# Performance work log

Hardware: AMD Instinct MI355X
Metric: run time of the kernel (lower is better)

## Reference

```python
import jax, jax.numpy as jnp
import numpy as np

# dims
B_, DM, DI, DS, DTR, DT_, G_, E_, K_, DC = 512, 1024, 2048, 64, 64, 64, 8, 4, 2, 4
# B_ batch, DM d_model, DI d_inner (expand*d_model), DS d_state, DTR dt_rank,
# DT_ D_time, G_ KAN grid size, E_ num_experts, K_ top_k, DC d_conv


def setup_inputs() -> dict:
    key = jax.random.key(0)
    ks = jax.random.split(key, 16)
    def n(i, shape, s=0.02):
        return jax.random.normal(ks[i], shape, dtype=jnp.float32) * s
    return {
        "uk_current_input": jax.random.normal(ks[0], (B_, DM), dtype=jnp.float32),
        "tk_current": jax.random.uniform(ks[1], (B_, 1), dtype=jnp.float32),
        "tk_previous": jax.random.uniform(ks[2], (B_, 1), dtype=jnp.float32),
        # input_proj
        "W_in": n(3, (DM, DM)), "b_in": jnp.zeros((DM,), jnp.float32),
        # K_MOTE router + sinusoidal time experts
        "router_W": n(4, (E_, 1), 1.0), "router_b": jnp.zeros((E_,), jnp.float32),
        "freq": jax.random.uniform(ks[5], (E_, DT_), minval=0.1, maxval=10.0),
        "phase": n(6, (E_, DT_), 1.0),
        "kan_W": n(7, (DT_, DT_, G_), 0.1),
        # Mamba SSM params
        "W_inproj": n(8, (2 * DI, DM)),
        "conv_w": n(9, (DI, DC), 0.1), "conv_b": jnp.zeros((DI,), jnp.float32),
        "W_x": n(10, (DTR + 2 * DS, DI)),
        "W_dt": n(11, (DI, DTR)), "dt_bias": jnp.full((DI,), -4.0, jnp.float32),
        "W_delta": n(12, (DI, DT_)),
        "A_log": jnp.log(jnp.tile(jnp.arange(1, DS + 1, dtype=jnp.float32), (DI, 1))),
        "D_skip": jnp.ones((DI,), jnp.float32),
        "W_out": n(13, (DM, DI)),
    }


def _k_mote(t, router_W, router_b, freq, phase):
    # t: (B,1) -> embedding (B, D_time), weights (B,E), mask (B,E)
    logits = t @ router_W.T + router_b                      # (B,E)
    w = jax.nn.softmax(logits, axis=-1)
    _, top_idx = jax.lax.top_k(w, K_)
    mask = jax.nn.one_hot(top_idx, E_, dtype=w.dtype).sum(axis=1)  # (B,E) binary
    w_sel = w * mask
    w_norm = w_sel / (w_sel.sum(axis=-1, keepdims=True) + 1e-8)
    # expert sinusoidal embeddings: (B,E,D_time)
    emb = jnp.sin(t[:, :, None] * freq[None] + phase[None])
    out = jnp.einsum('be,bed->bd', w_norm, emb)
    return out, w, mask


def _kan(x, kan_W):
    # rkhs_gaussian basis on fixed grid in [-1,1]
    grid = jnp.linspace(-1.0, 1.0, G_, dtype=x.dtype)
    h = 2.0 / (G_ - 1)
    phi = jnp.exp(-jnp.square((x[..., None] - grid) / h))   # (B, D_time, G)
    return jnp.einsum('big,oig->bo', phi, kan_W)


def _mamba_step(u, dt_emb, W_inproj, conv_w, conv_b, W_x, W_dt, dt_bias,
                W_delta, A_log, D_skip, W_out):
    # single-timestep selective scan (seq_len=1, zero initial state)
    xz = u @ W_inproj.T                                     # (B, 2*DI)
    x, z = jnp.split(xz, 2, axis=-1)
    # causal depthwise conv over a length-1 sequence with zero left-pad:
    # only the last kernel tap contributes
    x = x * conv_w[:, -1] + conv_b
    x = jax.nn.silu(x)
    x_dbl = x @ W_x.T                                       # (B, DTR+2*DS)
    dt_r = x_dbl[:, :DTR]
    Bmat = x_dbl[:, DTR:DTR + DS]                           # (B, DS)
    Cmat = x_dbl[:, DTR + DS:]                              # (B, DS)
    # dt modulated by the K-MOTE/KAN delta-time embedding
    dt = jax.nn.softplus(dt_r @ W_dt.T + dt_emb @ W_delta.T + dt_bias)  # (B, DI)
    # h_prev = 0 so exp(dt*A)*h_prev vanishes; h = (dt*B) * x
    h = (dt * x)[:, :, None] * Bmat[:, None, :]             # (B, DI, DS)
    y = jnp.einsum('bds,bs->bd', h, Cmat) + D_skip * x
    y = y * jax.nn.silu(z)
    return y @ W_out.T                                      # (B, DM)


def reference(uk_current_input, tk_current, tk_previous, W_in, b_in,
              router_W, router_b, freq, phase, kan_W, W_inproj, conv_w, conv_b,
              W_x, W_dt, dt_bias, W_delta, A_log, D_skip, W_out):
    processed_uk = uk_current_input @ W_in.T + b_in
    emb_tk, expert_weights, expert_mask = _k_mote(tk_current, router_W, router_b, freq, phase)
    emb_tk_prev, _, _ = _k_mote(tk_previous, router_W, router_b, freq, phase)
    delta_t_emb = _kan(emb_tk, kan_W) - _kan(emb_tk_prev, kan_W)
    hk = _mamba_step(processed_uk, delta_t_emb, W_inproj, conv_w, conv_b,
                     W_x, W_dt, dt_bias, W_delta, A_log, D_skip, W_out)
    return hk, expert_weights, expert_mask
```

## Files before the change

kernel.cpp:

```cpp
#include <hip/hip_runtime.h>
#include <hip/hip_bf16.h>
#include <math.h>

#define B_  512
#define DM  1024
#define DI  2048
#define DS  64
#define DTR 64
#define DT  64
#define G_  8
#define E_  4
#define DC  4

typedef __bf16 bf16x8 __attribute__((ext_vector_type(8)));
typedef float  f32x4  __attribute__((ext_vector_type(4)));
typedef unsigned short ushort_t;

__device__ __forceinline__ float bf2f(__hip_bfloat16 h) { return __bfloat162float(h); }
__device__ __forceinline__ __hip_bfloat16 f2bf(float f) { return __float2bfloat16(f); }
__device__ __forceinline__ float sigmoidf_(float x){ return 1.f/(1.f+expf(-x)); }
__device__ __forceinline__ float siluf_(float x){ return x*sigmoidf_(x); }
__device__ __forceinline__ float softplusf_(float x){ return (x>20.f)? x : log1pf(expf(x)); }

__device__ __forceinline__ unsigned int pack2(float a, float b) {
  unsigned short ua = __builtin_bit_cast(unsigned short, (__bf16)a);
  unsigned short ub = __builtin_bit_cast(unsigned short, (__bf16)b);
  return (unsigned int)ua | ((unsigned int)ub << 16);
}
__device__ __forceinline__ uint4 cvt8(float4 v0, float4 v1) {
  uint4 r;
  r.x = pack2(v0.x, v0.y); r.y = pack2(v0.z, v0.w);
  r.z = pack2(v1.x, v1.y); r.w = pack2(v1.z, v1.w);
  return r;
}

enum EpiKind { EPI_PART=0, EPI_G2=1, EPI_G4=2 };

struct KParams {
  const float *uk, *tk_c, *tk_p, *W_in, *b_in, *rW, *rb, *freq, *phase, *kanW;
  const float *W_inproj, *conv_w, *conv_b, *W_x, *W_dt, *dt_bias, *W_delta, *D_skip, *W_out;
  __hip_bfloat16 *Pu, *Xs, *Sz, *Yb, *Acat;
  __hip_bfloat16 *Wip_bf, *Wx_bf, *Wdt128, *Wout_bf;
  float *bc, *Part, *out_hk, *out_w, *out_mask;
};

__device__ __forceinline__ void cvt_chunk(const float* __restrict__ s,
                                          __hip_bfloat16* __restrict__ d)
{
  float4 v0 = *reinterpret_cast<const float4*>(s);
  float4 v1 = *reinterpret_cast<const float4*>(s + 4);
  *reinterpret_cast<uint4*>(d) = cvt8(v0, v1);
}

template<int BM, int BN, int WMT, int WNT, int EK, bool CVTA, bool CVTB>
__device__ __forceinline__ void gemm_tile(char* smemc, int bxi, int byi, int bzi,
    const void* __restrict__ Ap, const void* __restrict__ Bp,
    float* __restrict__ Coutp, int Ka, int Kb, int kLen, int N, const KParams& p)
{
  static_assert(BM == 32*WMT && BN == 32*WNT, "2x2 wave layout");
  constexpr int BK = 128, SA = 136;
  constexpr int NA = (BM*BK)/(256*8);
  constexpr int NB = (BN*BK)/(256*8);
  ushort_t* sA = (ushort_t*)smemc;
  ushort_t* sB = (ushort_t*)(smemc + (size_t)2*BM*SA*sizeof(ushort_t));
  const int tid  = threadIdx.x;
  const int wave = tid >> 6, lane = tid & 63;
  const int wm = wave >> 1, wn = wave & 1;
  const int r = lane & 15, q = lane >> 4;
  const int bm = byi * BM, bn = bxi * BN;
  const int kBase = bzi * kLen;
  const int T = kLen / BK;

  uint4 ua[NA], ub[NB];
  float4 fa[NA][2], fb[NB][2];

  auto loadTiles = [&](int k0) {
    #pragma unroll
    for (int c=0;c<NA;++c) {
      int idx = tid*8 + c*2048; int row = idx>>7, kk = idx&127;
      if constexpr (CVTA) {
        const float* s = (const float*)Ap + (size_t)(bm+row)*Ka + k0 + kk;
        fa[c][0] = *reinterpret_cast<const float4*>(s);
        fa[c][1] = *reinterpret_cast<const float4*>(s+4);
      } else {
        ua[c] = *reinterpret_cast<const uint4*>((const __hip_bfloat16*)Ap + (size_t)(bm+row)*Ka + k0 + kk);
      }
    }
    #pragma unroll
    for (int c=0;c<NB;++c) {
      int idx = tid*8 + c*2048; int row = idx>>7, kk = idx&127;
      if constexpr (CVTB) {
        const float* s = (const float*)Bp + (size_t)(bn+row)*Kb + k0 + kk;
        fb[c][0] = *reinterpret_cast<const float4*>(s);
        fb[c][1] = *reinterpret_cast<const float4*>(s+4);
      } else {
        ub[c] = *reinterpret_cast<const uint4*>((const __hip_bfloat16*)Bp + (size_t)(bn+row)*Kb + k0 + kk);
      }
    }
  };
  auto writeTiles = [&](int buf) {
    #pragma unroll
    for (int c=0;c<NA;++c) {
      int idx = tid*8 + c*2048; int row = idx>>7, kk = idx&127;
      uint4 v; if constexpr (CVTA) v = cvt8(fa[c][0], fa[c][1]); else v = ua[c];
      *reinterpret_cast<uint4*>(&sA[buf*(BM*SA) + row*SA + kk]) = v;
    }
    #pragma unroll
    for (int c=0;c<NB;++c) {
      int idx = tid*8 + c*2048; int row = idx>>7, kk = idx&127;
      uint4 v; if constexpr (CVTB) v = cvt8(fb[c][0], fb[c][1]); else v = ub[c];
      *reinterpret_cast<uint4*>(&sB[buf*(BN*SA) + row*SA + kk]) = v;
    }
  };

  f32x4 acc[WMT][WNT];
  #pragma unroll
  for (int i=0;i<WMT;++i)
    #pragma unroll
    for (int j=0;j<WNT;++j) acc[i][j] = (f32x4){0.f,0.f,0.f,0.f};

  loadTiles(kBase);
  writeTiles(0);
  for (int t=0; t<T; ++t) {
    __syncthreads();
    const int cur = t & 1;
    if (t+1 < T) loadTiles(kBase + (t+1)*BK);
    #pragma unroll
    for (int ks=0; ks<4; ++ks) {
      bf16x8 af[WMT], bfr[WNT];
      #pragma unroll
      for (int mt=0; mt<WMT; ++mt)
        af[mt] = *reinterpret_cast<const bf16x8*>(&sA[cur*(BM*SA) + (wm*(WMT*16)+mt*16+r)*SA + ks*32 + q*8]);
      #pragma unroll
      for (int nt=0; nt<WNT; ++nt)
        bfr[nt] = *reinterpret_cast<const bf16x8*>(&sB[cur*(BN*SA) + (wn*(WNT*16)+nt*16+r)*SA + ks*32 + q*8]);
      #pragma unroll
      for (int mt=0; mt<WMT; ++mt)
        #pragma unroll
        for (int nt=0; nt<WNT; ++nt)
          acc[mt][nt] = __builtin_amdgcn_mfma_f32_16x16x32_bf16(af[mt], bfr[nt], acc[mt][nt], 0,0,0);
    }
    if (t+1 < T) writeTiles(cur ^ 1);
  }

  #pragma unroll
  for (int mt=0; mt<WMT; ++mt) {
    #pragma unroll
    for (int nt=0; nt<WNT; ++nt) {
      #pragma unroll
      for (int i=0;i<4;++i) {
        int grow = bm + wm*(WMT*16) + mt*16 + q*4 + i;
        int gcol = bn + wn*(WNT*16) + nt*16 + r;
        float v = acc[mt][nt][i];
        if constexpr (EK == EPI_PART) {
          float* P = Coutp + (size_t)bzi * ((size_t)B_*N);
          P[(size_t)grow*N + gcol] = v;
        } else if constexpr (EK == EPI_G2) {
          if (gcol < DI) {
            float xc = v * p.conv_w[gcol*DC + (DC-1)] + p.conv_b[gcol];
            p.Xs[(size_t)grow*DI + gcol] = f2bf(siluf_(xc));
          } else {
            p.Sz[(size_t)grow*DI + (gcol - DI)] = f2bf(siluf_(v));
          }
        } else {
          float dt  = softplusf_(v + p.dt_bias[gcol]);
          float xsv = bf2f(p.Xs[(size_t)grow*DI + gcol]);
          float szv = bf2f(p.Sz[(size_t)grow*DI + gcol]);
          float y = (dt * xsv * p.bc[grow] + p.D_skip[gcol] * xsv) * szv;
          p.Yb[(size_t)grow*DI + gcol] = f2bf(y);
        }
      }
    }
  }
}


__device__ __forceinline__ void route(float t, const float* rW, const float* rb,
                                      float* w, float* mask, float* wn)
{
  float l[E_];
  float m = -1e30f;
  for (int e=0;e<E_;++e){ l[e] = t*rW[e] + rb[e]; m = fmaxf(m, l[e]); }
  float s = 0.f;
  for (int e=0;e<E_;++e){ w[e] = expf(l[e]-m); s += w[e]; }
  for (int e=0;e<E_;++e) w[e] /= s;
  int i1 = 0;
  for (int e=1;e<E_;++e) if (w[e] > w[i1]) i1 = e;
  int i2 = -1;
  for (int e=0;e<E_;++e) if (e != i1 && (i2 < 0 || w[e] > w[i2])) i2 = e;
  float ssel = w[i1] + w[i2] + 1e-8f;
  for (int e=0;e<E_;++e){
    float mk = (e==i1 || e==i2) ? 1.f : 0.f;
    mask[e] = mk;
    wn[e] = mk * w[e] / ssel;
  }
}

__device__ __forceinline__ void kan_job(char* smemc, int job, const KParams& p)
{
  float* dphi   = (float*)smemc;
  float* kchunk = dphi + 4*512;
  const int tid = threadIdx.x;
  const int wv = tid >> 6, lane = tid & 63;
  const int b = job*4 + wv;
  {
    float t  = p.tk_c[b];
    float tp = p.tk_p[b];
    float w_c[E_], mk_c[E_], wn_c[E_];
    float w_p[E_], mk_p[E_], wn_p[E_];
    route(t,  p.rW, p.rb, w_c, mk_c, wn_c);
    route(tp, p.rW, p.rb, w_p, mk_p, wn_p);
    if (lane < E_) {
      p.out_w[b*E_ + lane]    = w_c[lane];
      p.out_mask[b*E_ + lane] = mk_c[lane];
    }
    float ec = 0.f, epv = 0.f;
    #pragma unroll
    for (int e=0;e<E_;++e) {
      float f  = p.freq[e*DT + lane];
      float ph = p.phase[e*DT + lane];
      ec  += wn_c[e] * sinf(t*f + ph);
      epv += wn_p[e] * sinf(tp*f + ph);
    }
    const float h = 2.f/(G_-1);
    #pragma unroll
    for (int g=0; g<G_; ++g) {
      float gr = -1.f + g*h;
      float a  = (ec - gr)/h;
      float bb = (epv - gr)/h;
      dphi[wv*512 + lane*G_ + g] = expf(-a*a) - expf(-bb*bb);
    }
  }

  float accv = 0.f;
  #pragma unroll
  for (int c=0;c<4;++c) {
    __syncthreads();
    {
      const int rr = tid >> 2, seg = tid & 3;
      const float* src = p.kanW + (size_t)rr*512 + c*128 + seg*32;
      float* dst = kchunk + rr*132 + seg*32;
      #pragma unroll
      for (int i=0;i<8;++i)
        *reinterpret_cast<float4*>(dst + i*4) = *reinterpret_cast<const float4*>(src + i*4);
    }
    __syncthreads();
    const float* kr = kchunk + lane*132;
    const float* dd = dphi + wv*512 + c*128;
    #pragma unroll
    for (int j=0;j<128;j+=4) {
      float4 kv = *reinterpret_cast<const float4*>(kr + j);
      float4 dv = *reinterpret_cast<const float4*>(dd + j);
      accv += kv.x*dv.x + kv.y*dv.y + kv.z*dv.z + kv.w*dv.w;
    }
  }
  p.Acat[b*128 + 64 + lane] = f2bf(accv);
}


#define GEMM_SMEM(BM,BN) ((2*(BM)*136 + 2*(BN)*136)*2)

__global__ __launch_bounds__(256)
void g1kan_conv_kernel(KParams p)
{
  __shared__ __align__(16) char smem[GEMM_SMEM(32,64)];
  const int id = blockIdx.x, t = threadIdx.x;
  if (id < 128) {
    kan_job(smem, id, p);
  } else if (id < 1152) {
    const int id2 = id - 128;
    const int bxi = id2 & 15, byi = (id2 >> 4) & 15, bzi = id2 >> 8;
    gemm_tile<32,64,1,2,EPI_PART,true,true>(smem, bxi, byi, bzi,
        p.uk, p.W_in, p.Part, DM, DM, 256, DM, p);
  } else if (id < 3200) { size_t c = (size_t)(id-1152)*256 + t; cvt_chunk(p.W_inproj + c*8, p.Wip_bf  + c*8); }
  else if (id < 3392)   { size_t c = (size_t)(id-3200)*256 + t; cvt_chunk(p.W_x      + c*8, p.Wx_bf   + c*8); }
  else if (id < 4416)   { size_t c = (size_t)(id-3392)*256 + t; cvt_chunk(p.W_out    + c*8, p.Wout_bf + c*8); }
  else {                  size_t c = (size_t)(id-4416)*256 + t;
    int row = (int)(c >> 4), col0 = ((int)c & 15)*8;
    const float* s = (col0 < 64) ? (p.W_dt    + (size_t)row*64 + col0)
                                 : (p.W_delta + (size_t)row*64 + (col0-64));
    cvt_chunk(s, p.Wdt128 + (size_t)row*128 + col0);
  }
}

__global__ __launch_bounds__(256)
void g2_kernel(KParams p)
{
  __shared__ __align__(16) char smem[GEMM_SMEM(32,64)];
  const int bxi = blockIdx.x & 63, byi = blockIdx.x >> 6;
  gemm_tile<32,64,1,2,EPI_G2,false,false>(smem, bxi, byi, 0, p.Pu, p.Wip_bf, nullptr, DM, DM, DM, 2*DI, p);
}

__global__ __launch_bounds__(256)
void g3_kernel(KParams p)
{
  __shared__ __align__(16) char smem[GEMM_SMEM(32,64)];
  const int bxi = blockIdx.x % 3, rem = blockIdx.x / 3;
  const int byi = rem & 15, bzi = rem >> 4;
  gemm_tile<32,64,1,2,EPI_PART,false,false>(smem, bxi, byi, bzi, p.Xs, p.Wx_bf, p.Part, DI, DI, 256, 192, p);
}

__global__ __launch_bounds__(256)
void g4_kernel(KParams p)
{
  __shared__ __align__(16) char smem[GEMM_SMEM(32,64)];
  const int bxi = blockIdx.x & 31, byi = blockIdx.x >> 5;
  gemm_tile<32,64,1,2,EPI_G4,false,false>(smem, bxi, byi, 0, p.Acat, p.Wdt128, nullptr, 128, 128, 128, DI, p);
}

__global__ __launch_bounds__(256)
void g5_kernel(KParams p)
{
  __shared__ __align__(16) char smem[GEMM_SMEM(32,64)];
  const int bxi = blockIdx.x & 15, rem = blockIdx.x >> 4;
  const int byi = rem & 15, bzi = rem >> 4;
  gemm_tile<32,64,1,2,EPI_PART,false,false>(smem, bxi, byi, bzi, p.Yb, p.Wout_bf, p.Part, DI, DI, 512, DM, p);
}

__global__ __launch_bounds__(256)
void reduce_bias_kernel(KParams p)
{
  const int i = blockIdx.x*256 + threadIdx.x;
  const int total = B_*DM/4;
  const float4* pp = (const float4*)p.Part;
  float4 s = pp[i];
  #pragma unroll
  for (int k=1;k<4;++k){ float4 t = pp[i + k*total]; s.x+=t.x; s.y+=t.y; s.z+=t.z; s.w+=t.w; }
  float4 bv = ((const float4*)p.b_in)[i & (DM/4 - 1)];
  uint2 o; o.x = pack2(s.x+bv.x, s.y+bv.y); o.y = pack2(s.z+bv.z, s.w+bv.w);
  ((uint2*)p.Pu)[i] = o;
}

__global__ __launch_bounds__(192)
void reduce_g3_kernel(KParams p)
{
  const int row = blockIdx.x, col = threadIdx.x;
  const int stride = B_*192;
  float s = 0.f;
  #pragma unroll
  for (int k=0;k<8;++k) s += p.Part[(size_t)k*stride + row*192 + col];
  __shared__ float sBC[128];
  if (col < 64) p.Acat[row*128 + col] = f2bf(s);
  else          sBC[col-64] = s;
  __syncthreads();
  if (col < 64) {
    float pval = sBC[col] * sBC[col+64];
    #pragma unroll
    for (int off=32; off; off>>=1) pval += __shfl_down(pval, off);
    if (col == 0) p.bc[row] = pval;
  }
}

__global__ __launch_bounds__(256)
void reduce_plain_kernel(KParams p)
{
  const int i = blockIdx.x*256 + threadIdx.x;
  const int total = B_*DM/4;
  const float4* pp = (const float4*)p.Part;
  float4 s = pp[i];
  #pragma unroll
  for (int k=1;k<4;++k){ float4 t = pp[i + k*total]; s.x+=t.x; s.y+=t.y; s.z+=t.z; s.w+=t.w; }
  ((float4*)p.out_hk)[i] = s;
}

extern "C" void kernel_launch(void* const* d_in, const int* in_sizes, int n_in,
                              void* d_out, int out_size, void* d_ws, size_t ws_size,
                              hipStream_t stream)
{
  KParams p;
  p.uk       = (const float*)d_in[0];
  p.tk_c     = (const float*)d_in[1];
  p.tk_p     = (const float*)d_in[2];
  p.W_in     = (const float*)d_in[3];
  p.b_in     = (const float*)d_in[4];
  p.rW       = (const float*)d_in[5];
  p.rb       = (const float*)d_in[6];
  p.freq     = (const float*)d_in[7];
  p.phase    = (const float*)d_in[8];
  p.kanW     = (const float*)d_in[9];
  p.W_inproj = (const float*)d_in[10];
  p.conv_w   = (const float*)d_in[11];
  p.conv_b   = (const float*)d_in[12];
  p.W_x      = (const float*)d_in[13];
  p.W_dt     = (const float*)d_in[14];
  p.dt_bias  = (const float*)d_in[15];
  p.W_delta  = (const float*)d_in[16];
  p.D_skip   = (const float*)d_in[18];
  p.W_out    = (const float*)d_in[19];

  char* ws = (char*)d_ws;
  p.Pu     = (__hip_bfloat16*)(ws);
  p.Xs     = (__hip_bfloat16*)(ws + (size_t)(1<<20));
  p.Sz     = (__hip_bfloat16*)(ws + (size_t)3*(1<<20));
  p.Yb     = (__hip_bfloat16*)(ws + (size_t)5*(1<<20));
  p.Acat   = (__hip_bfloat16*)(ws + (size_t)7*(1<<20));
  p.bc     = (float*)         (ws + (size_t)7*(1<<20) + (128<<10));
  p.Part   = (float*)         (ws + (size_t)8*(1<<20));
  p.Wip_bf = (__hip_bfloat16*)(ws + (size_t)19*(1<<20));
  p.Wx_bf  = (__hip_bfloat16*)(ws + (size_t)27*(1<<20));
  p.Wdt128 = (__hip_bfloat16*)(ws + (size_t)28*(1<<20));
  p.Wout_bf= (__hip_bfloat16*)(ws + (size_t)29*(1<<20));

  p.out_hk   = (float*)d_out;
  p.out_w    = p.out_hk + (size_t)B_*DM;
  p.out_mask = p.out_w  + (size_t)B_*E_;

  g1kan_conv_kernel<<<dim3(4544), 256, 0, stream>>>(p);
  reduce_bias_kernel<<<dim3(512), 256, 0, stream>>>(p);

  g2_kernel<<<dim3(1024), 256, 0, stream>>>(p);

  g3_kernel<<<dim3(384), 256, 0, stream>>>(p);
  reduce_g3_kernel<<<dim3(512), 192, 0, stream>>>(p);

  g4_kernel<<<dim3(512), 256, 0, stream>>>(p);

  g5_kernel<<<dim3(1024), 256, 0, stream>>>(p);
  reduce_plain_kernel<<<dim3(512), 256, 0, stream>>>(p);
}
```

Before: 169.1 us.

## Drop split-K for first GEMM and fuse G3 reduction into G4 kernel

The W_in GEMM no longer uses split-K. Each of its 256 tiles runs the full K loop and writes bias-added bf16 directly, which removes the reduce_bias kernel and the partial-sum round trip. The G3 split-K reduction and the B·C dot product move into a rewritten G4 kernel that sums the partials into shared memory, computes bc per row, and runs a 32x128 MFMA tile with the Mamba epilogue. This removes two launches and a global intermediate. In exchange, G1 has less parallelism and longer per-block K loops, and each G4 block redoes the partial reduction for its rows across 16 column blocks.

```diff
diff --git a/kernel.cpp b/kernel.cpp
--- a/kernel.cpp
+++ b/kernel.cpp
@@ -34,7 +34,7 @@
   return r;
 }
 
-enum EpiKind { EPI_PART=0, EPI_G2=1, EPI_G4=2 };
+enum EpiKind { EPI_PART=0, EPI_G2=1, EPI_G4=2, EPI_BIAS=3 };
 
 struct KParams {
   const float *uk, *tk_c, *tk_p, *W_in, *b_in, *rW, *rb, *freq, *phase, *kanW;
@@ -155,6 +155,8 @@
         if constexpr (EK == EPI_PART) {
           float* P = Coutp + (size_t)bzi * ((size_t)B_*N);
           P[(size_t)grow*N + gcol] = v;
+        } else if constexpr (EK == EPI_BIAS) {
+          p.Pu[(size_t)grow*N + gcol] = f2bf(v + p.b_in[gcol]);
         } else if constexpr (EK == EPI_G2) {
           if (gcol < DI) {
             float xc = v * p.conv_w[gcol*DC + (DC-1)] + p.conv_b[gcol];
@@ -162,12 +164,6 @@
           } else {
             p.Sz[(size_t)grow*DI + (gcol - DI)] = f2bf(siluf_(v));
           }
-        } else {
-          float dt  = softplusf_(v + p.dt_bias[gcol]);
-          float xsv = bf2f(p.Xs[(size_t)grow*DI + gcol]);
-          float szv = bf2f(p.Sz[(size_t)grow*DI + gcol]);
-          float y = (dt * xsv * p.bc[grow] + p.D_skip[gcol] * xsv) * szv;
-          p.Yb[(size_t)grow*DI + gcol] = f2bf(y);
         }
       }
     }
@@ -267,15 +263,15 @@
   const int id = blockIdx.x, t = threadIdx.x;
   if (id < 128) {
     kan_job(smem, id, p);
-  } else if (id < 1152) {
+  } else if (id < 384) {
     const int id2 = id - 128;
-    const int bxi = id2 & 15, byi = (id2 >> 4) & 15, bzi = id2 >> 8;
-    gemm_tile<32,64,1,2,EPI_PART,true,true>(smem, bxi, byi, bzi,
-        p.uk, p.W_in, p.Part, DM, DM, 256, DM, p);
-  } else if (id < 3200) { size_t c = (size_t)(id-1152)*256 + t; cvt_chunk(p.W_inproj + c*8, p.Wip_bf  + c*8); }
-  else if (id < 3392)   { size_t c = (size_t)(id-3200)*256 + t; cvt_chunk(p.W_x      + c*8, p.Wx_bf   + c*8); }
-  else if (id < 4416)   { size_t c = (size_t)(id-3392)*256 + t; cvt_chunk(p.W_out    + c*8, p.Wout_bf + c*8); }
-  else {                  size_t c = (size_t)(id-4416)*256 + t;
+    const int bxi = id2 & 15, byi = id2 >> 4;
+    gemm_tile<32,64,1,2,EPI_BIAS,true,true>(smem, bxi, byi, 0,
+        p.uk, p.W_in, nullptr, DM, DM, DM, DM, p);
+  } else if (id < 2432) { size_t c = (size_t)(id-384)*256 + t;  cvt_chunk(p.W_inproj + c*8, p.Wip_bf  + c*8); }
+  else if (id < 2624)   { size_t c = (size_t)(id-2432)*256 + t; cvt_chunk(p.W_x      + c*8, p.Wx_bf   + c*8); }
+  else if (id < 3648)   { size_t c = (size_t)(id-2624)*256 + t; cvt_chunk(p.W_out    + c*8, p.Wout_bf + c*8); }
+  else {                  size_t c = (size_t)(id-3648)*256 + t;
     int row = (int)(c >> 4), col0 = ((int)c & 15)*8;
     const float* s = (col0 < 64) ? (p.W_dt    + (size_t)row*64 + col0)
                                  : (p.W_delta + (size_t)row*64 + (col0-64));
@@ -303,9 +299,95 @@
 __global__ __launch_bounds__(256)
 void g4_kernel(KParams p)
 {
-  __shared__ __align__(16) char smem[GEMM_SMEM(32,64)];
-  const int bxi = blockIdx.x & 31, byi = blockIdx.x >> 5;
-  gemm_tile<32,64,1,2,EPI_G4,false,false>(smem, bxi, byi, 0, p.Acat, p.Wdt128, nullptr, 128, 128, 128, DI, p);
+  __shared__ __align__(16) ushort_t sA4[32*136];
+  __shared__ __align__(16) ushort_t sB4[128*136];
+  __shared__ float sBcOut[32];
+  float* sBC = (float*)sB4;
+
+  const int tid = threadIdx.x;
+  const int byi = blockIdx.x & 15, bxi = blockIdx.x >> 4;
+  const int bm = byi*32, bn = bxi*128;
+
+  #pragma unroll
+  for (int c=0;c<6;++c) {
+    int f4id = tid + c*256;
+    int row = f4id / 48, cq = f4id % 48;
+    int col0 = cq*4;
+    const float* src = p.Part + (size_t)(bm+row)*192 + col0;
+    float4 s = {0.f,0.f,0.f,0.f};
+    #pragma unroll
+    for (int k=0;k<8;++k) {
+      float4 tv = *reinterpret_cast<const float4*>(src + (size_t)k*((size_t)B_*192));
+      s.x+=tv.x; s.y+=tv.y; s.z+=tv.z; s.w+=tv.w;
+    }
+    if (col0 < 64) {
+      uint2 o; o.x = pack2(s.x, s.y); o.y = pack2(s.z, s.w);
+      *reinterpret_cast<uint2*>(&sA4[row*136 + col0]) = o;
+    } else {
+      *reinterpret_cast<float4*>(&sBC[row*128 + (col0-64)]) = s;
+    }
+  }
+  {
+    int row = tid >> 3, c0 = (tid & 7)*8;
+    uint4 kv = *reinterpret_cast<const uint4*>(p.Acat + (size_t)(bm+row)*128 + 64 + c0);
+    *reinterpret_cast<uint4*>(&sA4[row*136 + 64 + c0]) = kv;
+  }
+  __syncthreads();
+
+  if (tid < 64) {
+    int row = tid >> 1, half = tid & 1;
+    const float* base = &sBC[row*128 + half*32];
+    float a = 0.f;
+    #pragma unroll
+    for (int j=0;j<8;++j) {
+      float4 bv = *reinterpret_cast<const float4*>(base + 4*j);
+      float4 cv = *reinterpret_cast<const float4*>(base + 64 + 4*j);
+      a += bv.x*cv.x + bv.y*cv.y + bv.z*cv.z + bv.w*cv.w;
+    }
+    a += __shfl_xor(a, 1);
+    if (half == 0) sBcOut[row] = a;
+  }
+  __syncthreads();
+
+  #pragma unroll
+  for (int c=0;c<8;++c) {
+    int e = tid + c*256;
+    int row = e >> 4, col0 = (e & 15)*8;
+    *reinterpret_cast<uint4*>(&sB4[row*136 + col0]) =
+        *reinterpret_cast<const uint4*>(p.Wdt128 + (size_t)(bn+row)*128 + col0);
+  }
+  __syncthreads();
+
+  const int wave = tid >> 6, lane = tid & 63;
+  const int wm = wave >> 1, wn = wave & 1;
+  const int r = lane & 15, q = lane >> 4;
+  f32x4 acc[4];
+  #pragma unroll
+  for (int nt=0;nt<4;++nt) acc[nt] = (f32x4){0.f,0.f,0.f,0.f};
+  #pragma unroll
+  for (int ks=0;ks<4;++ks) {
+    bf16x8 af = *reinterpret_cast<const bf16x8*>(&sA4[(wm*16+r)*136 + ks*32 + q*8]);
+    #pragma unroll
+    for (int nt=0;nt<4;++nt) {
+      bf16x8 bf = *reinterpret_cast<const bf16x8*>(&sB4[(wn*64+nt*16+r)*136 + ks*32 + q*8]);
+      acc[nt] = __builtin_amdgcn_mfma_f32_16x16x32_bf16(af, bf, acc[nt], 0,0,0);
+    }
+  }
+
+  #pragma unroll
+  for (int nt=0;nt<4;++nt) {
+    #pragma unroll
+    for (int i=0;i<4;++i) {
+      int lrow = wm*16 + q*4 + i;
+      int grow = bm + lrow;
+      int gcol = bn + wn*64 + nt*16 + r;
+      float dt  = softplusf_(acc[nt][i] + p.dt_bias[gcol]);
+      float xsv = bf2f(p.Xs[(size_t)grow*DI + gcol]);
+      float szv = bf2f(p.Sz[(size_t)grow*DI + gcol]);
+      float y = (dt * xsv * sBcOut[lrow] + p.D_skip[gcol] * xsv) * szv;
+      p.Yb[(size_t)grow*DI + gcol] = f2bf(y);
+    }
+  }
 }
 
 __global__ __launch_bounds__(256)
@@ -315,40 +397,6 @@
   const int bxi = blockIdx.x & 15, rem = blockIdx.x >> 4;
   const int byi = rem & 15, bzi = rem >> 4;
   gemm_tile<32,64,1,2,EPI_PART,false,false>(smem, bxi, byi, bzi, p.Yb, p.Wout_bf, p.Part, DI, DI, 512, DM, p);
-}
-
-__global__ __launch_bounds__(256)
-void reduce_bias_kernel(KParams p)
-{
-  const int i = blockIdx.x*256 + threadIdx.x;
-  const int total = B_*DM/4;
-  const float4* pp = (const float4*)p.Part;
-  float4 s = pp[i];
-  #pragma unroll
-  for (int k=1;k<4;++k){ float4 t = pp[i + k*total]; s.x+=t.x; s.y+=t.y; s.z+=t.z; s.w+=t.w; }
-  float4 bv = ((const float4*)p.b_in)[i & (DM/4 - 1)];
-  uint2 o; o.x = pack2(s.x+bv.x, s.y+bv.y); o.y = pack2(s.z+bv.z, s.w+bv.w);
-  ((uint2*)p.Pu)[i] = o;
-}
-
-__global__ __launch_bounds__(192)
-void reduce_g3_kernel(KParams p)
-{
-  const int row = blockIdx.x, col = threadIdx.x;
-  const int stride = B_*192;
-  float s = 0.f;
-  #pragma unroll
-  for (int k=0;k<8;++k) s += p.Part[(size_t)k*stride + row*192 + col];
-  __shared__ float sBC[128];
-  if (col < 64) p.Acat[row*128 + col] = f2bf(s);
-  else          sBC[col-64] = s;
-  __syncthreads();
-  if (col < 64) {
-    float pval = sBC[col] * sBC[col+64];
-    #pragma unroll
-    for (int off=32; off; off>>=1) pval += __shfl_down(pval, off);
-    if (col == 0) p.bc[row] = pval;
-  }
 }
 
 __global__ __launch_bounds__(256)
@@ -405,15 +453,12 @@
   p.out_w    = p.out_hk + (size_t)B_*DM;
   p.out_mask = p.out_w  + (size_t)B_*E_;
 
-  g1kan_conv_kernel<<<dim3(4544), 256, 0, stream>>>(p);
-  reduce_bias_kernel<<<dim3(512), 256, 0, stream>>>(p);
+  g1kan_conv_kernel<<<dim3(3776), 256, 0, stream>>>(p);
 
   g2_kernel<<<dim3(1024), 256, 0, stream>>>(p);
 
   g3_kernel<<<dim3(384), 256, 0, stream>>>(p);
-  reduce_g3_kernel<<<dim3(512), 192, 0, stream>>>(p);
-
-  g4_kernel<<<dim3(512), 256, 0, stream>>>(p);
+  g4_kernel<<<dim3(256), 256, 0, stream>>>(p);
 
   g5_kernel<<<dim3(1024), 256, 0, stream>>>(p);
   reduce_plain_kernel<<<dim3(512), 256, 0, stream>>>(p);
```

New measurement: 169.0 us. No clear change (-0.1%).
